# Kernel tuning notes

Hardware: AMD Instinct MI355X
Metric: run time of the kernel (lower is better)

## Reference

```python
import jax, jax.numpy as jnp
import numpy as np

B, C, H, W = 32, 512, 32, 32
N = H * W            # seq_len = 1024
HEADS = 8
DH = C // HEADS      # 64
K = 256              # linformer low-rank
EPS = 1e-5


def setup_inputs() -> dict:
    key = jax.random.key(0)
    ks = jax.random.split(key, 10)
    s = 0.02
    return {
        "x": jax.random.normal(ks[0], (B, C, H, W), dtype=jnp.float32),
        "pos": jax.random.normal(ks[1], (1, N, C), dtype=jnp.float32),
        "ln_g": jnp.ones((C,), dtype=jnp.float32),
        "ln_b": jnp.zeros((C,), dtype=jnp.float32),
        "Wq": jax.random.normal(ks[2], (C, C), dtype=jnp.float32) * s,
        "Wk": jax.random.normal(ks[3], (C, C), dtype=jnp.float32) * s,
        "Wv": jax.random.normal(ks[4], (C, C), dtype=jnp.float32) * s,
        "proj_k": jax.random.normal(ks[5], (N, K), dtype=jnp.float32) * s,
        "proj_v": jax.random.normal(ks[6], (N, K), dtype=jnp.float32) * s,
        "Wo": jax.random.normal(ks[7], (C, C), dtype=jnp.float32) * s,
        "bo": jnp.zeros((C,), dtype=jnp.float32),
    }


def reference(x, pos, ln_g, ln_b, Wq, Wk, Wv, proj_k, proj_v, Wo, bo):
    b, c, h, w = x.shape
    n = h * w
    # b c h w -> b (h w) c
    xf = x.reshape(b, c, n).transpose(0, 2, 1) + pos
    # LayerNorm (biased variance, eps=1e-5) + ReLU; dropout = identity (eval)
    mu = xf.mean(-1, keepdims=True)
    var = jnp.var(xf, axis=-1, keepdims=True)
    y = (xf - mu) * jax.lax.rsqrt(var + EPS) * ln_g + ln_b
    y = jax.nn.relu(y)
    # Linformer self-attention
    q = y @ Wq                                   # [b,n,c]
    k_ = jnp.einsum('bnd,nk->bkd', y @ Wk, proj_k)  # [b,K,c]
    v_ = jnp.einsum('bnd,nk->bkd', y @ Wv, proj_v)  # [b,K,c]
    q = q.reshape(b, n, HEADS, DH)
    k_ = k_.reshape(b, K, HEADS, DH)
    v_ = v_.reshape(b, K, HEADS, DH)
    dots = jnp.einsum('bnhd,bkhd->bhnk', q, k_) * (DH ** -0.5)
    attn = jax.nn.softmax(dots, axis=-1)
    out = jnp.einsum('bhnk,bkhd->bnhd', attn, v_).reshape(b, n, c)
    out = out @ Wo + bo
    # residual with (x + pos), then back to b c h w
    out = out + xf
    return out.transpose(0, 2, 1).reshape(b, c, h, w)
```

## Files before the change

kernel.cpp:

```cpp
#include <hip/hip_runtime.h>
#include <hip/hip_bf16.h>
#include <cstdint>

#define BB  32
#define CC  512
#define NN  1024
#define HH  8
#define DHH 64
#define KR  256

using f32x4  = __attribute__((ext_vector_type(4))) float;
using f32x16 = __attribute__((ext_vector_type(16))) float;
using bf16x8 = __attribute__((ext_vector_type(8))) __bf16;
using u32x4  = __attribute__((ext_vector_type(4))) unsigned int;

__device__ __forceinline__ unsigned short f2bf(float f) {
  unsigned int u = __float_as_uint(f);
  u += 0x7fffu + ((u >> 16) & 1u);
  return (unsigned short)(u >> 16);
}

__device__ __forceinline__ float bf2f(unsigned short u) {
  return __uint_as_float(((unsigned int)u) << 16);
}

__device__ __forceinline__ unsigned int pknat(float a, float b) {
  unsigned short ua = __builtin_bit_cast(unsigned short, (__bf16)a);
  unsigned short ub = __builtin_bit_cast(unsigned short, (__bf16)b);
  return (unsigned int)ua | ((unsigned int)ub << 16);
}

__device__ __forceinline__ void gload16(const void* gsrc, void* ldst) {
  __builtin_amdgcn_global_load_lds(
      (const __attribute__((address_space(1))) unsigned int*)gsrc,
      (__attribute__((address_space(3))) unsigned int*)ldst, 16, 0, 0);
}

__global__ __launch_bounds__(256) void transcvt_all(
    const float* __restrict__ w0, const float* __restrict__ w1,
    const float* __restrict__ w2, const float* __restrict__ w3,
    const float* __restrict__ p0, const float* __restrict__ p1,
    const float* __restrict__ pos,
    unsigned short* __restrict__ d0, unsigned short* __restrict__ d1,
    unsigned short* __restrict__ d2, unsigned short* __restrict__ d3,
    unsigned short* __restrict__ e0, unsigned short* __restrict__ e1,
    float* __restrict__ posT) {
  const int m = blockIdx.y;
  int idx = blockIdx.x * 256 + threadIdx.x;
  if (m == 6) {
    #pragma unroll
    for (int h = 0; h < 2; ++h) {
      int e = idx + h * 262144;
      int c = e >> 10, n = e & 1023;
      posT[e] = pos[(size_t)n * CC + c];
    }
    return;
  }
  const float* src = m==0?w0:m==1?w1:m==2?w2:m==3?w3:m==4?p0:p1;
  unsigned short* dst = m==0?d0:m==1?d1:m==2?d2:m==3?d3:m==4?e0:e1;
  if (m < 4) {
    int dr = idx & 511;
    int dc = idx >> 9;
    dst[idx] = f2bf(src[(size_t)dr * 512 + dc]);
  } else {
    int n = idx & 1023, kk = idx >> 10;
    dst[idx] = f2bf(src[(size_t)n * 256 + kk]);
  }
}

__global__ __launch_bounds__(256) void ln_relu_kernel(
    const float* __restrict__ x, const float* __restrict__ posT,
    const float* __restrict__ g, const float* __restrict__ bta,
    unsigned short* __restrict__ y, unsigned short* __restrict__ yT) {
  __shared__ unsigned short tile[512][20];
  __shared__ float smp[4][16][2];
  __shared__ float smu[16], srs[16];
  const int b = blockIdx.y, n0 = blockIdx.x * 16;
  const int tid = threadIdx.x;
  const int wave = tid >> 6, lane = tid & 63;
  const float* xb = x + (size_t)b * CC * NN;
  const int q4 = (tid & 3) * 4;
  const int cbase = tid >> 2;

  float s[4] = {0.f,0.f,0.f,0.f}, s2[4] = {0.f,0.f,0.f,0.f};
  #pragma unroll
  for (int i = 0; i < 8; ++i) {
    int c = cbase + i * 64;
    float4 v  = *reinterpret_cast<const float4*>(&xb  [(size_t)c * NN + n0 + q4]);
    float4 pv = *reinterpret_cast<const float4*>(&posT[(size_t)c * NN + n0 + q4]);
    float f0 = v.x + pv.x, f1 = v.y + pv.y, f2 = v.z + pv.z, f3 = v.w + pv.w;
    s[0] += f0; s2[0] += f0 * f0;
    s[1] += f1; s2[1] += f1 * f1;
    s[2] += f2; s2[2] += f2 * f2;
    s[3] += f3; s2[3] += f3 * f3;
    uint2 u; u.x = pknat(f0, f1); u.y = pknat(f2, f3);
    *reinterpret_cast<uint2*>(&tile[c][q4]) = u;
  }
  #pragma unroll
  for (int d = 4; d < 64; d <<= 1) {
    #pragma unroll
    for (int j = 0; j < 4; ++j) { s[j] += __shfl_xor(s[j], d); s2[j] += __shfl_xor(s2[j], d); }
  }
  if (lane < 4) {
    #pragma unroll
    for (int j = 0; j < 4; ++j) { smp[wave][lane * 4 + j][0] = s[j]; smp[wave][lane * 4 + j][1] = s2[j]; }
  }
  __syncthreads();

  if (tid < 16) {
    float ss  = smp[0][tid][0] + smp[1][tid][0] + smp[2][tid][0] + smp[3][tid][0];
    float ss2 = smp[0][tid][1] + smp[1][tid][1] + smp[2][tid][1] + smp[3][tid][1];
    float mu = ss * (1.f / 512.f);
    float var = ss2 * (1.f / 512.f) - mu * mu;
    smu[tid] = mu;
    srs[tid] = rsqrtf(var + 1e-5f);
  }
  __syncthreads();

  {
    const int nl = tid >> 4, t16 = tid & 15;
    const float mu = smu[nl], rs = srs[nl];
    unsigned short* yb = y + ((size_t)b * NN + n0 + nl) * CC;
    #pragma unroll
    for (int k = 0; k < 8; ++k) {
      int c0 = k * 64 + t16 * 4;
      float4 gv = *reinterpret_cast<const float4*>(&g[c0]);
      float4 bv = *reinterpret_cast<const float4*>(&bta[c0]);
      float o0 = (bf2f(tile[c0 + 0][nl]) - mu) * rs * gv.x + bv.x; o0 = o0 > 0.f ? o0 : 0.f;
      float o1 = (bf2f(tile[c0 + 1][nl]) - mu) * rs * gv.y + bv.y; o1 = o1 > 0.f ? o1 : 0.f;
      float o2 = (bf2f(tile[c0 + 2][nl]) - mu) * rs * gv.z + bv.z; o2 = o2 > 0.f ? o2 : 0.f;
      float o3 = (bf2f(tile[c0 + 3][nl]) - mu) * rs * gv.w + bv.w; o3 = o3 > 0.f ? o3 : 0.f;
      unsigned short b0 = f2bf(o0), b1 = f2bf(o1), b2 = f2bf(o2), b3 = f2bf(o3);
      uint2 u; u.x = (unsigned int)b0 | ((unsigned int)b1 << 16);
      u.y = (unsigned int)b2 | ((unsigned int)b3 << 16);
      *reinterpret_cast<uint2*>(&yb[c0]) = u;
      tile[c0 + 0][nl] = b0; tile[c0 + 1][nl] = b1;
      tile[c0 + 2][nl] = b2; tile[c0 + 3][nl] = b3;
    }
  }
  __syncthreads();

  unsigned short* ytb = yT + (size_t)b * CC * NN + n0;
  #pragma unroll
  for (int h2 = 0; h2 < 2; ++h2) {
    int cc = h2 * 256 + tid;
    uint2 a0 = *reinterpret_cast<const uint2*>(&tile[cc][0]);
    uint2 a1 = *reinterpret_cast<const uint2*>(&tile[cc][4]);
    uint2 a2 = *reinterpret_cast<const uint2*>(&tile[cc][8]);
    uint2 a3 = *reinterpret_cast<const uint2*>(&tile[cc][12]);
    uint4 w0; w0.x = a0.x; w0.y = a0.y; w0.z = a1.x; w0.w = a1.y;
    uint4 w1; w1.x = a2.x; w1.y = a2.y; w1.z = a3.x; w1.w = a3.y;
    *reinterpret_cast<uint4*>(&ytb[(size_t)cc * NN])     = w0;
    *reinterpret_cast<uint4*>(&ytb[(size_t)cc * NN + 8]) = w1;
  }
}

template <int MODE>
__global__ __launch_bounds__(256) void gemm_tn(
    const unsigned short* __restrict__ A, int lda, long long strideA,
    const unsigned short* __restrict__ Bt, int ldb, long long strideB,
    unsigned short* __restrict__ Cb, long long strideC,
    unsigned short* __restrict__ Cb2, long long strideC2,
    int Nn, int Kk, int TB,
    const float* __restrict__ xres, const float* __restrict__ posT,
    const float* __restrict__ bias, float* __restrict__ outF) {
  __shared__ __align__(16) unsigned short sh[24576];
  unsigned short* aL = sh;
  unsigned short* bL = sh + 12288;
  const int zb = blockIdx.z;
  int sel = 0, mb;
  if (MODE == 3) {
    sel = blockIdx.y >> 1;
    mb = ((blockIdx.y & 1) + sel * 2) * 128;
    if (sel == 1) Bt += (size_t)512 * 512;
  } else {
    mb = blockIdx.y * 128;
  }
  const int nb = blockIdx.x * 128;
  A  += (size_t)strideA * zb;
  Bt += (size_t)strideB * zb;
  Cb += (size_t)strideC * zb;
  if (MODE == 3) Cb2 += (size_t)strideC2 * zb;
  const int tid  = threadIdx.x;
  const int lane = tid & 63;
  const int wave = tid >> 6;
  const int wm = (wave >> 1) * 64, wn = (wave & 1) * 64;
  const int sr  = lane >> 2;
  const int scw = lane & 3;
  f32x4 acc[4][4] = {};

  auto stage = [&](int buf, int k0) {
    #pragma unroll
    for (int i = 0; i < 2; ++i) {
      int rbase = wave * 32 + i * 16;
      int row = rbase + sr;
      int ca = scw ^ ((row ^ (row >> 2)) & 3);
      gload16(&A [(size_t)(mb + row) * lda + k0 + ca * 8], &aL[buf * 4096 + rbase * 32]);
      gload16(&Bt[(size_t)(nb + row) * ldb + k0 + ca * 8], &bL[buf * 4096 + rbase * 32]);
    }
  };

  const int nt = Kk >> 5;
  stage(0, 0);
  stage(1, 32);
  asm volatile("s_waitcnt vmcnt(4)" ::: "memory");
  __builtin_amdgcn_s_barrier();
  __builtin_amdgcn_sched_barrier(0);

  int cbuf = 0;
  for (int t = 0; t < nt; ++t) {
    if (t + 2 < nt) stage(cbuf == 0 ? 2 : cbuf - 1, (t + 2) << 5);

    bf16x8 af[4], bfv[4];
    const int kc = lane >> 4;
    #pragma unroll
    for (int i = 0; i < 4; ++i) {
      int ra = wm + i * 16 + (lane & 15);
      int rb = wn + i * 16 + (lane & 15);
      af[i]  = *reinterpret_cast<const bf16x8*>(&aL[cbuf * 4096 + ra * 32 + (kc ^ ((ra ^ (ra >> 2)) & 3)) * 8]);
      bfv[i] = *reinterpret_cast<const bf16x8*>(&bL[cbuf * 4096 + rb * 32 + (kc ^ ((rb ^ (rb >> 2)) & 3)) * 8]);
    }
    #pragma unroll
    for (int i = 0; i < 4; ++i)
      #pragma unroll
      for (int j = 0; j < 4; ++j)
        acc[i][j] = __builtin_amdgcn_mfma_f32_16x16x32_bf16(af[i], bfv[j], acc[i][j], 0, 0, 0);

    if (t + 2 < nt)      { asm volatile("s_waitcnt vmcnt(4)" ::: "memory"); }
    else if (t + 1 < nt) { asm volatile("s_waitcnt vmcnt(0)" ::: "memory"); }
    if (t + 1 < nt) {
      __builtin_amdgcn_s_barrier();
      __builtin_amdgcn_sched_barrier(0);
    }
    cbuf = (cbuf == 2) ? 0 : cbuf + 1;
  }

  if (MODE == 2) {
    float* Ct = reinterpret_cast<float*>(sh);
    const int halfsel = wave >> 1;
    const int t0base = nb & 1023;
    const int bcell = nb >> 10;
    #pragma unroll
    for (int half = 0; half < 2; ++half) {
      __syncthreads();
      if (halfsel == half) {
        #pragma unroll
        for (int i = 0; i < 4; ++i) {
          int rloc = i * 16 + ((lane >> 4) << 2);
          #pragma unroll
          for (int j = 0; j < 4; ++j) {
            int cl = wn + j * 16 + (lane & 15);
            #pragma unroll
            for (int t = 0; t < 4; ++t)
              Ct[(rloc + t) * 132 + cl] = acc[i][j][t];
          }
        }
      }
      __syncthreads();
      #pragma unroll
      for (int p8 = 0; p8 < 8; ++p8) {
        int e = p8 * 256 + tid;
        int r = e >> 5, f4 = (e & 31) * 4;
        int c = mb + half * 64 + r;
        size_t base = ((size_t)bcell * CC + c) * NN + t0base + f4;
        float4 cv = *reinterpret_cast<const float4*>(&Ct[r * 132 + f4]);
        float4 xv = *reinterpret_cast<const float4*>(&xres[base]);
        float4 pv = *reinterpret_cast<const float4*>(&posT[(size_t)c * NN + t0base + f4]);
        float bc = bias[c];
        float4 ov;
        ov.x = cv.x + xv.x + pv.x + bc;
        ov.y = cv.y + xv.y + pv.y + bc;
        ov.z = cv.z + xv.z + pv.z + bc;
        ov.w = cv.w + xv.w + pv.w + bc;
        *reinterpret_cast<float4*>(&outF[base]) = ov;
      }
    }
  } else {
    const bool transp = (MODE == 1) || (MODE == 3 && sel == 1);
    auto Ct = (unsigned short (*)[136])sh;
    __syncthreads();
    #pragma unroll
    for (int i = 0; i < 4; ++i) {
      const int r0 = wm + i * 16 + ((lane >> 4) << 2);
      #pragma unroll
      for (int j = 0; j < 4; ++j) {
        const int cl = wn + j * 16 + (lane & 15);
        #pragma unroll
        for (int t = 0; t < 4; ++t) {
          if (!transp) Ct[r0 + t][cl] = f2bf(acc[i][j][t]);
          else         Ct[cl][r0 + t] = f2bf(acc[i][j][t]);
        }
      }
    }
    __syncthreads();
    const int rr = tid >> 4, ch = tid & 15;
    #pragma unroll
    for (int it = 0; it < 8; ++it) {
      const int r = it * 16 + rr;
      uint4 v = *reinterpret_cast<const uint4*>(&Ct[r][ch * 8]);
      if (!transp)
        *reinterpret_cast<uint4*>(&Cb[(size_t)(mb + r) * Nn + nb + ch * 8]) = v;
      else if (MODE == 1)
        *reinterpret_cast<uint4*>(&Cb[(size_t)(nb + r) * TB + mb + ch * 8]) = v;
      else
        *reinterpret_cast<uint4*>(&Cb2[(size_t)(nb + r) * TB + (mb - 256) + ch * 8]) = v;
    }
  }
}

__global__ __launch_bounds__(256, 2) void attn_kernel(
    const unsigned short* __restrict__ q,
    const unsigned short* __restrict__ kB,
    const unsigned short* __restrict__ vT,
    unsigned short* __restrict__ O) {
  __shared__ __align__(16) unsigned short smem[32768];
  const int wgid = blockIdx.x;
  const int grp  = wgid & 255;
  const int tg   = wgid >> 8;
  const int h = grp & 7, b = grp >> 3;
  const int wave = threadIdx.x >> 6, lane = threadIdx.x & 63;
  const int t32 = lane & 31, g2 = lane >> 5;
  const int tokb = tg * 128 + wave * 32;

  const unsigned short* qp = q + ((size_t)(b * NN + tokb + t32)) * CC + h * DHH + g2 * 8;
  bf16x8 qf[4];
  #pragma unroll
  for (int st = 0; st < 4; ++st)
    qf[st] = *reinterpret_cast<const bf16x8*>(qp + (size_t)st * 16);

  {
    const unsigned short* kb = kB + ((size_t)b * KR) * CC + h * DHH;
    const int r0w = wave * 64;
    #pragma unroll
    for (int i = 0; i < 8; ++i) {
      int row = r0w + i * 8 + (lane >> 3);
      int sc  = (lane & 7) ^ (row & 7);
      gload16(kb + (size_t)row * CC + sc * 8, &smem[(r0w + i * 8) * 64]);
    }
    const unsigned short* vb = vT + ((size_t)b * CC + h * DHH) * KR;
    const int v0w = wave * 16;
    #pragma unroll
    for (int i = 0; i < 8; ++i) {
      int row = v0w + i * 2 + (lane >> 5);
      int sc  = (lane & 31) ^ (row & 7);
      gload16(vb + (size_t)row * KR + sc * 8, &smem[16384 + (v0w + i * 2) * 256]);
    }
  }
  __syncthreads();

  f32x16 s8[8] = {};
  #pragma unroll
  for (int t8 = 0; t8 < 8; ++t8) {
    const int row = t8 * 32 + t32;
    #pragma unroll
    for (int st = 0; st < 4; ++st) {
      int ch = (2 * st + g2) ^ (row & 7);
      bf16x8 kf = *reinterpret_cast<const bf16x8*>(&smem[row * 64 + ch * 8]);
      s8[t8] = __builtin_amdgcn_mfma_f32_32x32x16_bf16(kf, qf[st], s8[t8], 0, 0, 0);
    }
  }

  float m = -1e30f;
  #pragma unroll
  for (int t8 = 0; t8 < 8; ++t8)
    #pragma unroll
    for (int r = 0; r < 16; ++r) m = fmaxf(m, s8[t8][r]);
  m = fmaxf(m, __shfl_xor(m, 32));
  const float cexp = 0.125f * 1.44269504088896f;
  float ls = 0.f;
  #pragma unroll
  for (int t8 = 0; t8 < 8; ++t8)
    #pragma unroll
    for (int r = 0; r < 16; ++r) {
      float p = __builtin_amdgcn_exp2f((s8[t8][r] - m) * cexp);
      s8[t8][r] = p;
      ls += p;
    }
  ls += __shfl_xor(ls, 32);
  float rinv = __builtin_amdgcn_rcpf(ls);

  f32x16 o0 = {}, o1 = {};
  #pragma unroll
  for (int t8 = 0; t8 < 8; ++t8) {
    unsigned int pkd[8];
    #pragma unroll
    for (int qq = 0; qq < 4; ++qq) {
      pkd[qq * 2 + 0] = pknat(s8[t8][4 * qq + 0], s8[t8][4 * qq + 1]);
      pkd[qq * 2 + 1] = pknat(s8[t8][4 * qq + 2], s8[t8][4 * qq + 3]);
    }
    #pragma unroll
    for (int a = 0; a < 2; ++a) {
      const int ks = t8 * 2 + a;
      unsigned int xe0 = pkd[4 * a + 0], xe1 = pkd[4 * a + 1];
      unsigned int xo0 = pkd[4 * a + 2], xo1 = pkd[4 * a + 3];
      unsigned int d0 = g2 ? __shfl_xor(xo0, 32) : xe0;
      unsigned int d1 = g2 ? __shfl_xor(xo1, 32) : xe1;
      unsigned int d2 = g2 ? xo0 : __shfl_xor(xe0, 32);
      unsigned int d3 = g2 ? xo1 : __shfl_xor(xe1, 32);
      u32x4 pv_ = {d0, d1, d2, d3};
      bf16x8 pa = __builtin_bit_cast(bf16x8, pv_);
      #pragma unroll
      for (int dt = 0; dt < 2; ++dt) {
        int row = dt * 32 + t32;
        int ch = (2 * ks + g2) ^ (row & 7);
        bf16x8 bv = *reinterpret_cast<const bf16x8*>(&smem[16384 + row * 256 + ch * 8]);
        if (dt == 0) o0 = __builtin_amdgcn_mfma_f32_32x32x16_bf16(pa, bv, o0, 0, 0, 0);
        else         o1 = __builtin_amdgcn_mfma_f32_32x32x16_bf16(pa, bv, o1, 0, 0, 0);
      }
    }
  }

  unsigned short* Ob = O + ((size_t)(b * NN + tokb)) * CC + h * DHH;
  #pragma unroll
  for (int r = 0; r < 16; ++r) {
    int tl = (r & 3) + 8 * (r >> 2) + 4 * g2;
    float rs = __shfl(rinv, tl);
    Ob[(size_t)tl * CC + t32]      = f2bf(o0[r] * rs);
    Ob[(size_t)tl * CC + 32 + t32] = f2bf(o1[r] * rs);
  }
}

extern "C" void kernel_launch(void* const* d_in, const int* in_sizes, int n_in,
                              void* d_out, int out_size, void* d_ws, size_t ws_size,
                              hipStream_t stream) {
  const float* x    = (const float*)d_in[0];
  const float* pos  = (const float*)d_in[1];
  const float* ln_g = (const float*)d_in[2];
  const float* ln_b = (const float*)d_in[3];
  const float* Wq   = (const float*)d_in[4];
  const float* Wk   = (const float*)d_in[5];
  const float* Wv   = (const float*)d_in[6];
  const float* pk   = (const float*)d_in[7];
  const float* pv   = (const float*)d_in[8];
  const float* Wo   = (const float*)d_in[9];
  const float* bo   = (const float*)d_in[10];
  float* out = (float*)d_out;

  unsigned short* ws = (unsigned short*)d_ws;
  size_t off = 0;
  auto alloc = [&](size_t elems) { unsigned short* p = ws + off; off += elems; return p; };
  unsigned short* WqT     = alloc(512 * 512);
  unsigned short* WkT     = alloc(512 * 512);
  unsigned short* WvT     = alloc(512 * 512);
  unsigned short* WoT     = alloc(512 * 512);
  unsigned short* projcat = alloc((size_t)512 * 1024);
  float*          posTb   = (float*)alloc((size_t)512 * 1024 * 2);
  unsigned short* yB      = alloc((size_t)32768 * 512);
  unsigned short* yT      = alloc((size_t)32 * 512 * 1024);
  unsigned short* qB      = alloc((size_t)32768 * 512);
  unsigned short* zB      = alloc((size_t)32 * 512 * 512);
  unsigned short* kBuf    = alloc((size_t)32 * 256 * 512);
  unsigned short* vTB     = alloc((size_t)32 * 512 * 256);
  unsigned short* OB      = alloc((size_t)32768 * 512);

  transcvt_all<<<dim3(1024, 7), 256, 0, stream>>>(
      Wq, Wk, Wv, Wo, pk, pv, pos,
      WqT, WkT, WvT, WoT, projcat, projcat + (size_t)256 * 1024, posTb);

  ln_relu_kernel<<<dim3(64, 32), 256, 0, stream>>>(x, posTb, ln_g, ln_b, yB, yT);

  gemm_tn<0><<<dim3(4, 256), 256, 0, stream>>>(
      yB, 512, 0, WqT, 512, 0, qB, 0, nullptr, 0,
      512, 512, 0, nullptr, nullptr, nullptr, nullptr);

  gemm_tn<0><<<dim3(4, 4, 32), 256, 0, stream>>>(
      projcat, 1024, 0, yT, 1024, (long long)512 * 1024, zB, (long long)512 * 512,
      nullptr, 0, 512, 1024, 0, nullptr, nullptr, nullptr, nullptr);

  gemm_tn<3><<<dim3(4, 4, 32), 256, 0, stream>>>(
      zB, 512, (long long)512 * 512, WkT, 512, 0, kBuf, (long long)256 * 512,
      vTB, (long long)512 * 256, 512, 512, 256, nullptr, nullptr, nullptr, nullptr);

  attn_kernel<<<dim3(2048, 1, 1), 256, 0, stream>>>(qB, kBuf, vTB, OB);

  gemm_tn<2><<<dim3(256, 4), 256, 0, stream>>>(
      WoT, 512, 0, OB, 512, 0, nullptr, 0, nullptr, 0,
      32768, 512, 0, x, posTb, bo, out);
}
```

Baseline: 209.5 us.

## Process 64 tokens per LayerNorm block with token-major LDS tile

The LayerNorm+ReLU kernel now handles 64 tokens per 512-thread block instead of 16 tokens per 256 threads, using a token-major shared tile. The aim is wider, more coalesced writes of the transposed yT output (128-byte rows instead of 32-byte fragments) and vectorized 16-byte stores of the row-major output. In exchange it uses about 68KB of LDS per block, scalar 2-byte LDS scatter writes that may bank-conflict, and launches only 512 blocks, which can lower occupancy.

```diff
diff --git a/kernel.cpp b/kernel.cpp
--- a/kernel.cpp
+++ b/kernel.cpp
@@ -68,48 +68,68 @@
   }
 }
 
-__global__ __launch_bounds__(256) void ln_relu_kernel(
+__global__ __launch_bounds__(512) void ln_relu_kernel(
     const float* __restrict__ x, const float* __restrict__ posT,
     const float* __restrict__ g, const float* __restrict__ bta,
     unsigned short* __restrict__ y, unsigned short* __restrict__ yT) {
-  __shared__ unsigned short tile[512][20];
-  __shared__ float smp[4][16][2];
-  __shared__ float smu[16], srs[16];
-  const int b = blockIdx.y, n0 = blockIdx.x * 16;
+  __shared__ unsigned short tile[64][532];
+  __shared__ float smp[8][64][2];
+  __shared__ float smu[64], srs[64];
+  const int b = blockIdx.y, n0 = blockIdx.x * 64;
   const int tid = threadIdx.x;
-  const int wave = tid >> 6, lane = tid & 63;
-  const float* xb = x + (size_t)b * CC * NN;
-  const int q4 = (tid & 3) * 4;
-  const int cbase = tid >> 2;
-
-  float s[4] = {0.f,0.f,0.f,0.f}, s2[4] = {0.f,0.f,0.f,0.f};
+  const int wv = tid >> 6, ln_ = tid & 63;
+  const int q = ln_ & 7;
+  const int rrow = tid >> 3;
+  const float* xb = x    + (size_t)b * CC * NN + n0;
+  const float* pb = posT + n0;
+
+  float s[2][4] = {{0.f,0.f,0.f,0.f},{0.f,0.f,0.f,0.f}};
+  float s2[2][4] = {{0.f,0.f,0.f,0.f},{0.f,0.f,0.f,0.f}};
   #pragma unroll
   for (int i = 0; i < 8; ++i) {
-    int c = cbase + i * 64;
-    float4 v  = *reinterpret_cast<const float4*>(&xb  [(size_t)c * NN + n0 + q4]);
-    float4 pv = *reinterpret_cast<const float4*>(&posT[(size_t)c * NN + n0 + q4]);
-    float f0 = v.x + pv.x, f1 = v.y + pv.y, f2 = v.z + pv.z, f3 = v.w + pv.w;
-    s[0] += f0; s2[0] += f0 * f0;
-    s[1] += f1; s2[1] += f1 * f1;
-    s[2] += f2; s2[2] += f2 * f2;
-    s[3] += f3; s2[3] += f3 * f3;
-    uint2 u; u.x = pknat(f0, f1); u.y = pknat(f2, f3);
-    *reinterpret_cast<uint2*>(&tile[c][q4]) = u;
-  }
-  #pragma unroll
-  for (int d = 4; d < 64; d <<= 1) {
-    #pragma unroll
-    for (int j = 0; j < 4; ++j) { s[j] += __shfl_xor(s[j], d); s2[j] += __shfl_xor(s2[j], d); }
-  }
-  if (lane < 4) {
-    #pragma unroll
-    for (int j = 0; j < 4; ++j) { smp[wave][lane * 4 + j][0] = s[j]; smp[wave][lane * 4 + j][1] = s2[j]; }
+    const int c = i * 64 + rrow;
+    #pragma unroll
+    for (int j = 0; j < 2; ++j) {
+      const int t4 = q * 4 + j * 32;
+      float4 v  = *reinterpret_cast<const float4*>(&xb[(size_t)c * NN + t4]);
+      float4 pv = *reinterpret_cast<const float4*>(&pb[(size_t)c * NN + t4]);
+      float f0 = v.x + pv.x, f1 = v.y + pv.y;
+      float f2 = v.z + pv.z, f3 = v.w + pv.w;
+      s[j][0] += f0; s2[j][0] += f0 * f0;
+      s[j][1] += f1; s2[j][1] += f1 * f1;
+      s[j][2] += f2; s2[j][2] += f2 * f2;
+      s[j][3] += f3; s2[j][3] += f3 * f3;
+      tile[t4 + 0][c] = f2bf(f0);
+      tile[t4 + 1][c] = f2bf(f1);
+      tile[t4 + 2][c] = f2bf(f2);
+      tile[t4 + 3][c] = f2bf(f3);
+    }
+  }
+  #pragma unroll
+  for (int d = 8; d < 64; d <<= 1) {
+    #pragma unroll
+    for (int j = 0; j < 2; ++j)
+      #pragma unroll
+      for (int k = 0; k < 4; ++k) {
+        s[j][k]  += __shfl_xor(s[j][k],  d, 64);
+        s2[j][k] += __shfl_xor(s2[j][k], d, 64);
+      }
+  }
+  if (ln_ < 8) {
+    #pragma unroll
+    for (int j = 0; j < 2; ++j)
+      #pragma unroll
+      for (int k = 0; k < 4; ++k) {
+        smp[wv][ln_ * 4 + k + 32 * j][0] = s[j][k];
+        smp[wv][ln_ * 4 + k + 32 * j][1] = s2[j][k];
+      }
   }
   __syncthreads();
 
-  if (tid < 16) {
-    float ss  = smp[0][tid][0] + smp[1][tid][0] + smp[2][tid][0] + smp[3][tid][0];
-    float ss2 = smp[0][tid][1] + smp[1][tid][1] + smp[2][tid][1] + smp[3][tid][1];
+  if (tid < 64) {
+    float ss = 0.f, ss2 = 0.f;
+    #pragma unroll
+    for (int w = 0; w < 8; ++w) { ss += smp[w][tid][0]; ss2 += smp[w][tid][1]; }
     float mu = ss * (1.f / 512.f);
     float var = ss2 * (1.f / 512.f) - mu * mu;
     smu[tid] = mu;
@@ -118,40 +138,53 @@
   __syncthreads();
 
   {
-    const int nl = tid >> 4, t16 = tid & 15;
-    const float mu = smu[nl], rs = srs[nl];
-    unsigned short* yb = y + ((size_t)b * NN + n0 + nl) * CC;
-    #pragma unroll
-    for (int k = 0; k < 8; ++k) {
-      int c0 = k * 64 + t16 * 4;
-      float4 gv = *reinterpret_cast<const float4*>(&g[c0]);
-      float4 bv = *reinterpret_cast<const float4*>(&bta[c0]);
-      float o0 = (bf2f(tile[c0 + 0][nl]) - mu) * rs * gv.x + bv.x; o0 = o0 > 0.f ? o0 : 0.f;
-      float o1 = (bf2f(tile[c0 + 1][nl]) - mu) * rs * gv.y + bv.y; o1 = o1 > 0.f ? o1 : 0.f;
-      float o2 = (bf2f(tile[c0 + 2][nl]) - mu) * rs * gv.z + bv.z; o2 = o2 > 0.f ? o2 : 0.f;
-      float o3 = (bf2f(tile[c0 + 3][nl]) - mu) * rs * gv.w + bv.w; o3 = o3 > 0.f ? o3 : 0.f;
-      unsigned short b0 = f2bf(o0), b1 = f2bf(o1), b2 = f2bf(o2), b3 = f2bf(o3);
-      uint2 u; u.x = (unsigned int)b0 | ((unsigned int)b1 << 16);
-      u.y = (unsigned int)b2 | ((unsigned int)b3 << 16);
-      *reinterpret_cast<uint2*>(&yb[c0]) = u;
-      tile[c0 + 0][nl] = b0; tile[c0 + 1][nl] = b1;
-      tile[c0 + 2][nl] = b2; tile[c0 + 3][nl] = b3;
+    const int tok = ln_, ch = wv;
+    const float mu = smu[tok], rs = srs[tok];
+    unsigned short* yb = y + ((size_t)b * NN + n0 + tok) * CC + ch * 64;
+    #pragma unroll
+    for (int k = 0; k < 4; ++k) {
+      unsigned int out[8];
+      #pragma unroll
+      for (int m = 0; m < 4; ++m) {
+        const int c = ch * 64 + k * 16 + m * 4;
+        uint2 u = *reinterpret_cast<const uint2*>(&tile[tok][c]);
+        float4 gv = *reinterpret_cast<const float4*>(&g[c]);
+        float4 bv = *reinterpret_cast<const float4*>(&bta[c]);
+        float o0 = (bf2f((unsigned short)(u.x & 0xffff)) - mu) * rs * gv.x + bv.x;
+        float o1 = (bf2f((unsigned short)(u.x >> 16))    - mu) * rs * gv.y + bv.y;
+        float o2 = (bf2f((unsigned short)(u.y & 0xffff)) - mu) * rs * gv.z + bv.z;
+        float o3 = (bf2f((unsigned short)(u.y >> 16))    - mu) * rs * gv.w + bv.w;
+        o0 = o0 > 0.f ? o0 : 0.f;
+        o1 = o1 > 0.f ? o1 : 0.f;
+        o2 = o2 > 0.f ? o2 : 0.f;
+        o3 = o3 > 0.f ? o3 : 0.f;
+        unsigned int lo = pknat(o0, o1), hi = pknat(o2, o3);
+        out[m * 2] = lo; out[m * 2 + 1] = hi;
+        uint2 wbk; wbk.x = lo; wbk.y = hi;
+        *reinterpret_cast<uint2*>(&tile[tok][c]) = wbk;
+      }
+      uint4 w0; w0.x = out[0]; w0.y = out[1]; w0.z = out[2]; w0.w = out[3];
+      uint4 w1; w1.x = out[4]; w1.y = out[5]; w1.z = out[6]; w1.w = out[7];
+      *reinterpret_cast<uint4*>(&yb[k * 16])     = w0;
+      *reinterpret_cast<uint4*>(&yb[k * 16 + 8]) = w1;
     }
   }
   __syncthreads();
 
-  unsigned short* ytb = yT + (size_t)b * CC * NN + n0;
-  #pragma unroll
-  for (int h2 = 0; h2 < 2; ++h2) {
-    int cc = h2 * 256 + tid;
-    uint2 a0 = *reinterpret_cast<const uint2*>(&tile[cc][0]);
-    uint2 a1 = *reinterpret_cast<const uint2*>(&tile[cc][4]);
-    uint2 a2 = *reinterpret_cast<const uint2*>(&tile[cc][8]);
-    uint2 a3 = *reinterpret_cast<const uint2*>(&tile[cc][12]);
-    uint4 w0; w0.x = a0.x; w0.y = a0.y; w0.z = a1.x; w0.w = a1.y;
-    uint4 w1; w1.x = a2.x; w1.y = a2.y; w1.z = a3.x; w1.w = a3.y;
-    *reinterpret_cast<uint4*>(&ytb[(size_t)cc * NN])     = w0;
-    *reinterpret_cast<uint4*>(&ytb[(size_t)cc * NN + 8]) = w1;
+  {
+    const int c = tid;
+    unsigned short* ytb = yT + (size_t)b * CC * NN + (size_t)c * NN + n0;
+    unsigned int pk2[32];
+    #pragma unroll
+    for (int to = 0; to < 32; ++to)
+      pk2[to] = (unsigned int)tile[2 * to][c] | ((unsigned int)tile[2 * to + 1][c] << 16);
+    #pragma unroll
+    for (int v4 = 0; v4 < 8; ++v4) {
+      uint4 w;
+      w.x = pk2[v4 * 4 + 0]; w.y = pk2[v4 * 4 + 1];
+      w.z = pk2[v4 * 4 + 2]; w.w = pk2[v4 * 4 + 3];
+      *reinterpret_cast<uint4*>(&ytb[v4 * 8]) = w;
+    }
   }
 }
 
@@ -457,7 +490,7 @@
       Wq, Wk, Wv, Wo, pk, pv, pos,
       WqT, WkT, WvT, WoT, projcat, projcat + (size_t)256 * 1024, posTb);
 
-  ln_relu_kernel<<<dim3(64, 32), 256, 0, stream>>>(x, posTb, ln_g, ln_b, yB, yT);
+  ln_relu_kernel<<<dim3(16, 32), 512, 0, stream>>>(x, posTb, ln_g, ln_b, yB, yT);
 
   gemm_tn<0><<<dim3(4, 256), 256, 0, stream>>>(
       yB, 512, 0, WqT, 512, 0, qB, 0, nullptr, 0,
```

New measurement: 202.4 us. 3.3% less time.
